# Performance work log

Measured on AMD Instinct MI355X. Metric: run time of the kernel, lower is better.

The kernel has to match this reference:

```python
import jax, jax.numpy as jnp
import numpy as np

B, C, IC, H, W = 4, 256, 128, 64, 64
EPS = 1e-5  # BatchNorm eps (eval mode, running stats)


def conv_bn(x, w, b, gamma, beta, mean, var, relu):
    # 1x1 conv == channel contraction; BN in eval mode (affine w/ running stats)
    y = jnp.einsum('oc,bchw->bohw', w, x) + b[None, :, None, None]
    scale = gamma * jax.lax.rsqrt(var + EPS)
    shift = beta - mean * scale
    y = y * scale[None, :, None, None] + shift[None, :, None, None]
    return jax.nn.relu(y) if relu else y


def setup_inputs() -> dict:
    key = jax.random.key(0)
    ks = jax.random.split(key, 32)

    def branch(i, co, ci):
        return dict(
            w=jax.random.normal(ks[i], (co, ci), jnp.float32) * 0.05,
            b=jax.random.normal(ks[i + 1], (co,), jnp.float32) * 0.05,
            gamma=jax.random.uniform(ks[i + 2], (co,), jnp.float32, 0.5, 1.5),
            beta=jax.random.normal(ks[i + 3], (co,), jnp.float32) * 0.05,
            mean=jax.random.normal(ks[i + 4], (co,), jnp.float32) * 0.05,
            var=jax.random.uniform(ks[i + 5], (co,), jnp.float32, 0.5, 1.5),
        )

    g = branch(0, IC, C)
    th = branch(6, IC, C)
    ph = branch(12, IC, C)
    wo = branch(18, C, IC)
    inp = {'x': jax.random.normal(ks[24], (B, C, H, W), jnp.float32)}
    for pre, p in (('g', g), ('th', th), ('ph', ph), ('w', wo)):
        for k, v in p.items():
            inp[f'{pre}_{k}'] = v
    return inp


def reference(x, g_w, g_b, g_gamma, g_beta, g_mean, g_var,
              th_w, th_b, th_gamma, th_beta, th_mean, th_var,
              ph_w, ph_b, ph_gamma, ph_beta, ph_mean, ph_var,
              w_w, w_b, w_gamma, w_beta, w_mean, w_var):
    b, c, h, w = x.shape
    ic = g_w.shape[0]
    g_x = conv_bn(x, g_w, g_b, g_gamma, g_beta, g_mean, g_var, True).reshape(b, ic, h * w)     # [b,ic,n]
    theta = conv_bn(x, th_w, th_b, th_gamma, th_beta, th_mean, th_var, True).reshape(b, ic, h * w)
    phi = conv_bn(x, ph_w, ph_b, ph_gamma, ph_beta, ph_mean, ph_var, True).reshape(b, ic, h * w)
    # unscaled attention over flattened spatial positions
    f = jnp.einsum('bcn,bcm->bnm', theta, phi)     # [b,n,n]
    a = jax.nn.softmax(f, axis=2)
    y = jnp.einsum('bnm,bcm->bcn', a, g_x)         # [b,ic,n]
    y = y.reshape(b, ic, h, w)
    y = conv_bn(y, w_w, w_b, w_gamma, w_beta, w_mean, w_var, False)
    return y + x
```

## Files before the change

kernel.cpp:

```cpp
#include <hip/hip_runtime.h>
#include <math.h>

typedef __attribute__((ext_vector_type(8))) short short8;
typedef __attribute__((ext_vector_type(8))) _Float16 half8;
typedef __attribute__((ext_vector_type(4))) float f32x4;

#define NSP 4096
#define CIN 256
#define ICH 128
#define SPLITS 4
#define TILES_PER_SPLIT 16
#define LOG2E 1.44269504088896f

__device__ __forceinline__ unsigned short f2h(float x){
  union { _Float16 h; unsigned short u; } v; v.h = (_Float16)x; return v.u;
}
__device__ __forceinline__ float h2f(unsigned short u){
  union { _Float16 h; unsigned short u; } v; v.u = u; return (float)v.h;
}
__device__ __forceinline__ unsigned pk2h(float a, float b){
  union { __fp16 __attribute__((ext_vector_type(2))) v; unsigned u; } r;
  r.v = __builtin_amdgcn_cvt_pkrtz(a, b);
  return r.u;
}
__device__ __forceinline__ float fexp2(float x){
  float r;
  asm("v_exp_f32 %0, %1" : "=v"(r) : "v"(x));
  return r;
}
__device__ __forceinline__ int swz(int row, int e){ return e ^ ((row & 7) << 3); }

__device__ __forceinline__ f32x4 mfmah(short8 a, short8 b, f32x4 c){
  union { short8 s; half8 h; } ua, ub; ua.s = a; ub.s = b;
  return __builtin_amdgcn_mfma_f32_16x16x32_f16(ua.h, ub.h, c, 0, 0, 0);
}

__device__ __forceinline__ void st4h(unsigned short* p, unsigned short a, unsigned short b,
                                     unsigned short c, unsigned short d){
  ushort4 v; v.x=a; v.y=b; v.z=c; v.w=d;
  *(ushort4*)p = v;
}

__device__ __forceinline__ void gload_lds16(const unsigned short* g, unsigned short* l){
  __builtin_amdgcn_global_load_lds(
      (const __attribute__((address_space(1))) unsigned int*)g,
      (__attribute__((address_space(3))) unsigned int*)l, 16, 0, 0);
}

__device__ __forceinline__ void stage_nc(const unsigned short* gbase, unsigned short* lds,
                                         int w, int l){
  #pragma unroll
  for (int i=0;i<4;++i){
    int rl = 16*w + 4*i + (l>>4);
    int eg = ((l&15)*8) ^ ((rl&7)<<3);
    gload_lds16(gbase + (size_t)rl*128 + eg, lds + w*2048 + i*512);
  }
}

__device__ __forceinline__ int kperm(int q){
  return ((q>>4)&1)*4 + ((q>>2)&3)*8 + (q&3);
}

__global__ __launch_bounds__(256) void conv_fused_k(
    const float* __restrict__ x,
    const float* __restrict__ w0, const float* __restrict__ b0,
    const float* __restrict__ ga0, const float* __restrict__ be0,
    const float* __restrict__ me0, const float* __restrict__ va0,
    const float* __restrict__ w1, const float* __restrict__ b1,
    const float* __restrict__ ga1, const float* __restrict__ be1,
    const float* __restrict__ me1, const float* __restrict__ va1,
    const float* __restrict__ w2, const float* __restrict__ b2,
    const float* __restrict__ ga2, const float* __restrict__ be2,
    const float* __restrict__ me2, const float* __restrict__ va2,
    unsigned short* __restrict__ outg, unsigned short* __restrict__ outt,
    unsigned short* __restrict__ outp)
{
  const int b = blockIdx.z, nt = blockIdx.x, ot = blockIdx.y;
  const int n0 = nt*64, o0 = ot*64;
  const int t = threadIdx.x, w = t>>6, l = t&63;
  __shared__ unsigned short xs[64][64];
  __shared__ unsigned short ws[3][64][64];
  __shared__ float sc_s[3][64], sh_s[3][64];
  if (t < 64){
    int o = o0 + t;
    float s0 = ga0[o]*rsqrtf(va0[o]+1e-5f);
    sc_s[0][t]=s0; sh_s[0][t]=be0[o]-me0[o]*s0+b0[o]*s0;
    float s1 = ga1[o]*rsqrtf(va1[o]+1e-5f);
    sc_s[1][t]=s1*LOG2E; sh_s[1][t]=(be1[o]-me1[o]*s1+b1[o]*s1)*LOG2E;
    float s2 = ga2[o]*rsqrtf(va2[o]+1e-5f);
    sc_s[2][t]=s2; sh_s[2][t]=be2[o]-me2[o]*s2+b2[o]*s2;
  }
  const f32x4 Z = {0.f,0.f,0.f,0.f};
  f32x4 acc[3][4];
  #pragma unroll
  for (int br=0;br<3;++br) for (int i=0;i<4;++i) acc[br][i] = Z;
  const float* Wt[3] = {w0, w1, w2};

  for (int kc = 0; kc < CIN; kc += 64){
    __syncthreads();
    #pragma unroll
    for (int p = 0; p < 4; ++p){
      int cw = p*16 + (t>>4);
      int q4 = (t&15)*4;
      float4 xv = *(const float4*)(x + ((size_t)b*CIN + kc + cw)*NSP + n0 + q4);
      float xa[4] = {xv.x, xv.y, xv.z, xv.w};
      #pragma unroll
      for (int i=0;i<4;++i){
        int r = q4 + i;
        xs[r][swz(r, cw)] = f2h(xa[i]);
      }
      #pragma unroll
      for (int br=0;br<3;++br){
        float4 wv = *(const float4*)(Wt[br] + (size_t)(o0 + cw)*CIN + kc + q4);
        int cs = swz(cw, q4);
        st4h(&ws[br][cw][cs], f2h(wv.x), f2h(wv.y), f2h(wv.z), f2h(wv.w));
      }
    }
    __syncthreads();
    #pragma unroll
    for (int kf = 0; kf < 2; ++kf){
      int ko = kf*32 + (l>>4)*8;
      int wr = 16*w + (l&15);
      short8 wf0 = *(const short8*)&ws[0][wr][swz(wr, ko)];
      short8 wf1 = *(const short8*)&ws[1][wr][swz(wr, ko)];
      short8 wf2 = *(const short8*)&ws[2][wr][swz(wr, ko)];
      #pragma unroll
      for (int nf = 0; nf < 4; ++nf){
        int xr = 16*nf + (l&15);
        short8 xf = *(const short8*)&xs[xr][swz(xr, ko)];
        acc[0][nf] = mfmah(wf0, xf, acc[0][nf]);
        acc[1][nf] = mfmah(xf, wf1, acc[1][nf]);
        acc[2][nf] = mfmah(xf, wf2, acc[2][nf]);
      }
    }
  }
  #pragma unroll
  for (int j=0;j<4;++j){
    int ol = 16*w + (l>>4)*4 + j;
    float s = sc_s[0][ol], sh = sh_s[0][ol];
    #pragma unroll
    for (int nf=0;nf<4;++nf){
      int n = n0 + 16*nf + (l&15);
      int nst = (n & ~31) | kperm(n & 31);
      float v = fmaxf(acc[0][nf][j]*s + sh, 0.f);
      outg[((size_t)b*ICH + o0 + ol)*NSP + nst] = f2h(v);
    }
  }
  {
    int ol = 16*w + (l&15);
    float s1 = sc_s[1][ol], sh1 = sh_s[1][ol];
    float s2 = sc_s[2][ol], sh2 = sh_s[2][ol];
    #pragma unroll
    for (int nf=0; nf<4; ++nf)
      #pragma unroll
      for (int j=0;j<4;++j){
        int n = n0 + 16*nf + (l>>4)*4 + j;
        float v1 = fmaxf(acc[1][nf][j]*s1 + sh1, 0.f);
        float v2 = fmaxf(acc[2][nf][j]*s2 + sh2, 0.f);
        outt[((size_t)b*NSP + n)*ICH + o0 + ol] = f2h(v1);
        outp[((size_t)b*NSP + n)*ICH + o0 + ol] = f2h(v2);
      }
  }
}

__global__ __launch_bounds__(256, 2) void attn_k(
  const unsigned short* __restrict__ thp, const unsigned short* __restrict__ php,
  const unsigned short* __restrict__ gb, unsigned short* __restrict__ ypart,
  float* __restrict__ ml)
{
  const int bx = blockIdx.x;
  const int xcd = bx & 7, jj = bx >> 3;
  const int combo = xcd*2 + (jj>>5);
  const int qt = jj & 31;
  const int b = combo & 3, s = combo >> 2;
  const int n0 = qt*128;
  const int t = threadIdx.x, w = t>>6, l = t&63;

  __shared__ unsigned short kb[2][64][128];
  __shared__ unsigned short vb[2][128][64];

  stage_nc(thp + ((size_t)b*NSP + n0      )*ICH, &kb[0][0][0], w, l);
  stage_nc(thp + ((size_t)b*NSP + n0 + 64 )*ICH, &kb[1][0][0], w, l);
  __syncthreads();
  short8 qf0[4], qf1[4];
  {
    int qr = 16*w + (l&15);
    #pragma unroll
    for (int kf=0;kf<4;++kf){
      int ko = kf*32 + (l>>4)*8;
      qf0[kf] = *(const short8*)&kb[0][qr][swz(qr, ko)];
      qf1[kf] = *(const short8*)&kb[1][qr][swz(qr, ko)];
    }
  }
  __syncthreads();

  const f32x4 Z = {0.f,0.f,0.f,0.f};
  f32x4 oa0[8], oa1[8];
  #pragma unroll
  for (int i=0;i<8;++i){ oa0[i]=Z; oa1[i]=Z; }
  float m0r = -1e30f, m1r = -1e30f;
  float l0r = 0.f, l1r = 0.f;
  unsigned pk0[8], pk1[8];

  const int tile0 = s*TILES_PER_SPLIT;

  const unsigned short* kp[4];
  const unsigned short* vp[4];
  {
    const unsigned short* kbase = php + ((size_t)b*NSP + tile0*64)*ICH;
    const unsigned short* vbase = gb + (size_t)b*ICH*NSP + tile0*64;
    #pragma unroll
    for (int i=0;i<4;++i){
      int rl = 16*w + 4*i + (l>>4);
      int eg = ((l&15)*8) ^ ((rl&7)<<3);
      kp[i] = kbase + (size_t)rl*128 + eg;
      int cl = 32*w + 8*i + (l>>3);
      int me = ((l&7)*8) ^ ((cl&7)<<3);
      vp[i] = vbase + (size_t)cl*NSP + me;
    }
  }
  {
    unsigned short* kd = &kb[0][0][0] + w*2048;
    unsigned short* vd = &vb[0][0][0] + w*2048;
    #pragma unroll
    for (int i=0;i<4;++i){
      gload_lds16(kp[i], kd + i*512); kp[i] += 64*ICH;
      gload_lds16(vp[i], vd + i*512); vp[i] += 64;
    }
  }
  __syncthreads();
  int cur = 0;

  for (int it = 0; it < TILES_PER_SPLIT; ++it){
    if (it < TILES_PER_SPLIT-1){
      unsigned short* kd = &kb[cur^1][0][0] + w*2048;
      unsigned short* vd = &vb[cur^1][0][0] + w*2048;
      #pragma unroll
      for (int i=0;i<4;++i){
        gload_lds16(kp[i], kd + i*512); kp[i] += 64*ICH;
        gload_lds16(vp[i], vd + i*512); vp[i] += 64;
      }
    }

    f32x4 f0[4], f1[4];
    #pragma unroll
    for (int i=0;i<4;++i){ f0[i]=Z; f1[i]=Z; }
    __builtin_amdgcn_s_setprio(1);
    #pragma unroll
    for (int mf=0; mf<4; ++mf){
      int kr = 16*mf + (l&15);
      #pragma unroll
      for (int kf=0; kf<4; ++kf){
        short8 bh = *(const short8*)&kb[cur][kr][swz(kr, kf*32 + (l>>4)*8)];
        f0[mf] = mfmah(bh, qf0[kf], f0[mf]);
        f1[mf] = mfmah(bh, qf1[kf], f1[mf]);
      }
    }
    __builtin_amdgcn_s_setprio(0);

    #pragma unroll
    for (int h=0; h<2; ++h){
      f32x4* f = h ? f1 : f0;
      float& mr = h ? m1r : m0r;
      float& lr = h ? l1r : l0r;
      f32x4* oa = h ? oa1 : oa0;
      unsigned* pk = h ? pk1 : pk0;
      float a0 = fmaxf(fmaxf(f[0][0], f[0][1]), fmaxf(f[0][2], f[0][3]));
      float a1 = fmaxf(fmaxf(f[1][0], f[1][1]), fmaxf(f[1][2], f[1][3]));
      float a2 = fmaxf(fmaxf(f[2][0], f[2][1]), fmaxf(f[2][2], f[2][3]));
      float a3 = fmaxf(fmaxf(f[3][0], f[3][1]), fmaxf(f[3][2], f[3][3]));
      float mx = fmaxf(fmaxf(a0, a1), fmaxf(a2, a3));
      mx = fmaxf(mx, __shfl_xor(mx, 16));
      mx = fmaxf(mx, __shfl_xor(mx, 32));
      if (__any(mx - mr > 11.5f)){
        float mn = fmaxf(mr, mx);
        float al = fexp2(mr - mn);
        mr = mn; lr *= al;
        #pragma unroll
        for (int j=0;j<4;++j){
          float alj = __shfl(al, (l>>4)*4 + j);
          #pragma unroll
          for (int cf=0;cf<8;++cf) oa[cf][j] *= alj;
        }
      }
      float s0 = 0.f, s1 = 0.f, s2 = 0.f, s3 = 0.f;
      #pragma unroll
      for (int mf=0;mf<4;++mf){
        float p0 = fexp2(f[mf][0] - mr);
        float p1 = fexp2(f[mf][1] - mr);
        float p2 = fexp2(f[mf][2] - mr);
        float p3 = fexp2(f[mf][3] - mr);
        pk[2*mf+0] = pk2h(p0, p1);
        pk[2*mf+1] = pk2h(p2, p3);
        s0 += p0; s1 += p1; s2 += p2; s3 += p3;
      }
      lr += (s0 + s1) + (s2 + s3);
    }

    __builtin_amdgcn_s_setprio(1);
    {
      int g8 = (l>>4)*8;
      #pragma unroll
      for (int mk=0;mk<2;++mk){
        union { unsigned u[4]; short8 s8; } a0u, a1u;
        #pragma unroll
        for (int q=0;q<4;++q){ a0u.u[q] = pk0[4*mk+q]; a1u.u[q] = pk1[4*mk+q]; }
        #pragma unroll
        for (int cf=0;cf<8;++cf){
          int vr = 16*cf + (l&15);
          short8 bv = *(const short8*)&vb[cur][vr][swz(vr, mk*32 + g8)];
          oa0[cf] = mfmah(a0u.s8, bv, oa0[cf]);
          oa1[cf] = mfmah(a1u.s8, bv, oa1[cf]);
        }
      }
    }
    __builtin_amdgcn_s_setprio(0);

    __syncthreads();
    cur ^= 1;
  }

  #pragma unroll
  for (int h=0; h<2; ++h){
    float mr = h ? m1r : m0r;
    float lr = h ? l1r : l0r;
    f32x4* oa = h ? oa1 : oa0;
    lr += __shfl_xor(lr, 16);
    lr += __shfl_xor(lr, 32);
    float invl = 1.f / lr;
    #pragma unroll
    for (int j=0;j<4;++j){
      float inv = __shfl(invl, (l>>4)*4 + j);
      int n = n0 + h*64 + 16*w + (l>>4)*4 + j;
      #pragma unroll
      for (int cf=0;cf<8;++cf){
        int c = 16*cf + (l&15);
        ypart[(((size_t)s*4 + b)*NSP + n)*ICH + c] = f2h(oa[cf][j]*inv);
      }
    }
    if (l < 16){
      int n = n0 + h*64 + 16*w + l;
      ml[(((size_t)s*4 + b)*NSP + n)*2 + 0] = mr;
      ml[(((size_t)s*4 + b)*NSP + n)*2 + 1] = lr;
    }
  }
}

__global__ __launch_bounds__(256) void final_k(
  const unsigned short* __restrict__ ypart, const float* __restrict__ ml,
  const float* __restrict__ x, const float* __restrict__ Wm,
  const float* __restrict__ bias, const float* __restrict__ gamma,
  const float* __restrict__ beta, const float* __restrict__ mean,
  const float* __restrict__ var, float* __restrict__ out)
{
  const int b = blockIdx.z, ot = blockIdx.y, nt = blockIdx.x;
  const int n0 = nt*64, o0 = ot*64;
  const int t = threadIdx.x, w = t>>6, l = t&63;
  __shared__ unsigned short ys[64][128];
  __shared__ unsigned short w2s[64][128];
  __shared__ float wc[SPLITS][64];
  __shared__ float sc_s[64], sh_s[64];
  if (t < 64){
    int o = o0 + t;
    float s = gamma[o]*rsqrtf(var[o]+1e-5f);
    sc_s[t]=s; sh_s[t]=beta[o]-mean[o]*s+bias[o]*s;
  } else if (t < 128){
    int r = t - 64, n = n0 + r;
    float mv[SPLITS], lv[SPLITS];
    #pragma unroll
    for (int s=0;s<SPLITS;++s){
      mv[s] = ml[(((size_t)s*4 + b)*NSP + n)*2 + 0];
      lv[s] = ml[(((size_t)s*4 + b)*NSP + n)*2 + 1];
    }
    float M = fmaxf(fmaxf(mv[0],mv[1]), fmaxf(mv[2],mv[3]));
    float wsum = 0.f, wv[SPLITS];
    #pragma unroll
    for (int s=0;s<SPLITS;++s){ wv[s] = lv[s]*exp2f(mv[s]-M); wsum += wv[s]; }
    float inv = 1.f/wsum;
    #pragma unroll
    for (int s=0;s<SPLITS;++s) wc[s][r] = wv[s]*inv;
  }
  __syncthreads();
  #pragma unroll
  for (int p=0;p<4;++p){
    int id = p*256 + t, r = id>>4, c8 = (id&15)*8;
    float accv[8] = {0,0,0,0,0,0,0,0};
    #pragma unroll
    for (int s=0;s<SPLITS;++s){
      short8 v = *(const short8*)(ypart + (((size_t)s*4 + b)*NSP + n0 + r)*ICH + c8);
      float wgt = wc[s][r];
      #pragma unroll
      for (int i=0;i<8;++i) accv[i] += wgt * h2f(((unsigned short*)&v)[i]);
    }
    unsigned short hv[8];
    #pragma unroll
    for (int i=0;i<8;++i) hv[i] = f2h(accv[i]);
    *(short8*)&ys[r][swz(r,c8)] = *(short8*)hv;

    float4 u0 = *(const float4*)(Wm + (size_t)(o0 + r)*ICH + c8);
    float4 u1 = *(const float4*)(Wm + (size_t)(o0 + r)*ICH + c8 + 4);
    unsigned short wh[8] = {f2h(u0.x),f2h(u0.y),f2h(u0.z),f2h(u0.w),
                            f2h(u1.x),f2h(u1.y),f2h(u1.z),f2h(u1.w)};
    *(short8*)&w2s[r][swz(r,c8)] = *(short8*)wh;
  }
  __syncthreads();
  const f32x4 Z = {0.f,0.f,0.f,0.f};
  f32x4 acc[4];
  for (int i=0;i<4;++i) acc[i]=Z;
  #pragma unroll
  for (int kf=0;kf<4;++kf){
    int ko = kf*32 + (l>>4)*8;
    int wr = 16*w + (l&15);
    short8 a = *(const short8*)&w2s[wr][swz(wr,ko)];
    #pragma unroll
    for (int nf=0;nf<4;++nf){
      int yr = 16*nf + (l&15);
      short8 bb = *(const short8*)&ys[yr][swz(yr,ko)];
      acc[nf] = mfmah(a, bb, acc[nf]);
    }
  }
  #pragma unroll
  for (int j=0;j<4;++j){
    int ol = 16*w + (l>>4)*4 + j;
    float s = sc_s[ol], sh = sh_s[ol];
    #pragma unroll
    for (int nf=0;nf<4;++nf){
      int n = n0 + 16*nf + (l&15);
      size_t idx = ((size_t)b*CIN + o0 + ol)*NSP + n;
      out[idx] = acc[nf][j]*s + sh + x[idx];
    }
  }
}

extern "C" void kernel_launch(void* const* d_in, const int* in_sizes, int n_in,
                              void* d_out, int out_size, void* d_ws, size_t ws_size,
                              hipStream_t stream){
  const float* x    = (const float*)d_in[0];
  const float* g_w  = (const float*)d_in[1];
  const float* g_b  = (const float*)d_in[2];
  const float* g_ga = (const float*)d_in[3];
  const float* g_be = (const float*)d_in[4];
  const float* g_me = (const float*)d_in[5];
  const float* g_va = (const float*)d_in[6];
  const float* t_w  = (const float*)d_in[7];
  const float* t_b  = (const float*)d_in[8];
  const float* t_ga = (const float*)d_in[9];
  const float* t_be = (const float*)d_in[10];
  const float* t_me = (const float*)d_in[11];
  const float* t_va = (const float*)d_in[12];
  const float* p_w  = (const float*)d_in[13];
  const float* p_b  = (const float*)d_in[14];
  const float* p_ga = (const float*)d_in[15];
  const float* p_be = (const float*)d_in[16];
  const float* p_me = (const float*)d_in[17];
  const float* p_va = (const float*)d_in[18];
  const float* w_w  = (const float*)d_in[19];
  const float* w_b  = (const float*)d_in[20];
  const float* w_ga = (const float*)d_in[21];
  const float* w_be = (const float*)d_in[22];
  const float* w_me = (const float*)d_in[23];
  const float* w_va = (const float*)d_in[24];

  char* ws = (char*)d_ws;
  const size_t SEG = (size_t)4*NSP*ICH*sizeof(unsigned short);
  unsigned short* th_t  = (unsigned short*)(ws);
  unsigned short* ph_t  = (unsigned short*)(ws + SEG);
  unsigned short* g_cn  = (unsigned short*)(ws + 2*SEG);
  unsigned short* ypart = (unsigned short*)(ws + 3*SEG);
  float*          mlb   = (float*)(ws + 3*SEG + SPLITS*SEG);

  dim3 blk(256,1,1);
  conv_fused_k<<<dim3(64,2,4), blk, 0, stream>>>(
      x,
      g_w, g_b, g_ga, g_be, g_me, g_va,
      t_w, t_b, t_ga, t_be, t_me, t_va,
      p_w, p_b, p_ga, p_be, p_me, p_va,
      g_cn, th_t, ph_t);
  attn_k<<<dim3(512,1,1), blk, 0, stream>>>(th_t, ph_t, g_cn, ypart, mlb);
  final_k<<<dim3(64,4,4), blk, 0, stream>>>(ypart, mlb, x, w_w, w_b, w_ga, w_be, w_me, w_va, (float*)d_out);
}
```

Baseline: 71.34 us.

## Template attention kernel on waves per block; use 8-wave blocks with 8 KV splits

The attention kernel is parameterized by waves per block. With enough workspace it launches 512 blocks of 512 threads, each covering 256 query rows and an 8-way split of the key sequence, so each block runs 8 tiles instead of 16. The final combine kernel is templated on the split count so it can merge 8 partial results. More splits and larger blocks mean each K/V tile staged in LDS serves twice as many query rows and the grid carries more waves, at the cost of double the partial-output traffic and a heavier combine step.

```diff
diff --git a/kernel.cpp b/kernel.cpp
--- a/kernel.cpp
+++ b/kernel.cpp
@@ -8,8 +8,6 @@
 #define NSP 4096
 #define CIN 256
 #define ICH 128
-#define SPLITS 4
-#define TILES_PER_SPLIT 16
 #define LOG2E 1.44269504088896f
 
 __device__ __forceinline__ unsigned short f2h(float x){
@@ -45,16 +43,6 @@
   __builtin_amdgcn_global_load_lds(
       (const __attribute__((address_space(1))) unsigned int*)g,
       (__attribute__((address_space(3))) unsigned int*)l, 16, 0, 0);
-}
-
-__device__ __forceinline__ void stage_nc(const unsigned short* gbase, unsigned short* lds,
-                                         int w, int l){
-  #pragma unroll
-  for (int i=0;i<4;++i){
-    int rl = 16*w + 4*i + (l>>4);
-    int eg = ((l&15)*8) ^ ((rl&7)<<3);
-    gload_lds16(gbase + (size_t)rl*128 + eg, lds + w*2048 + i*512);
-  }
 }
 
 __device__ __forceinline__ int kperm(int q){
@@ -163,33 +151,62 @@
   }
 }
 
-__global__ __launch_bounds__(256, 2) void attn_k(
+template<int WPB>
+__global__ __launch_bounds__(WPB*64, WPB/2) void attn_k(
   const unsigned short* __restrict__ thp, const unsigned short* __restrict__ php,
   const unsigned short* __restrict__ gb, unsigned short* __restrict__ ypart,
   float* __restrict__ ml)
 {
+  constexpr int QROWS = WPB*32;
+  constexpr int HBLK  = WPB*16;
+  constexpr int TPS   = 64/WPB;
+  constexpr int QTC   = 128/WPB;
+  constexpr int NLD   = 16/WPB;
+
   const int bx = blockIdx.x;
   const int xcd = bx & 7, jj = bx >> 3;
-  const int combo = xcd*2 + (jj>>5);
-  const int qt = jj & 31;
+  const int combo = xcd*(WPB/2) + jj/QTC;
+  const int qt = jj % QTC;
   const int b = combo & 3, s = combo >> 2;
-  const int n0 = qt*128;
+  const int n0 = qt*QROWS;
   const int t = threadIdx.x, w = t>>6, l = t&63;
 
-  __shared__ unsigned short kb[2][64][128];
-  __shared__ unsigned short vb[2][128][64];
-
-  stage_nc(thp + ((size_t)b*NSP + n0      )*ICH, &kb[0][0][0], w, l);
-  stage_nc(thp + ((size_t)b*NSP + n0 + 64 )*ICH, &kb[1][0][0], w, l);
+  __shared__ unsigned short kbuf[2][8192];
+  __shared__ unsigned short vbuf[2][8192];
+
+  unsigned short* kb0 = kbuf[0];
+  unsigned short* kb1 = kbuf[1];
+  unsigned short* vb0 = vbuf[0];
+  unsigned short* vb1 = vbuf[1];
+  auto qsel = [&](int c) -> unsigned short* {
+    return c==0 ? kb0 : (c==1 ? kb1 : (c==2 ? vb0 : vb1));
+  };
+
+  #pragma unroll
+  for (int c=0;c<WPB/2;++c){
+    const unsigned short* src = thp + ((size_t)b*NSP + n0 + c*64)*ICH;
+    unsigned short* dst = qsel(c) + w*(NLD*512);
+    #pragma unroll
+    for (int i=0;i<NLD;++i){
+      int rl = (64/WPB)*w + 4*i + (l>>4);
+      int eg = ((l&15)*8) ^ ((rl&7)<<3);
+      gload_lds16(src + (size_t)rl*128 + eg, dst + i*512);
+    }
+  }
   __syncthreads();
   short8 qf0[4], qf1[4];
   {
-    int qr = 16*w + (l&15);
+    int base0 = 16*w;
+    int c0 = base0>>6, r0 = (base0&63) + (l&15);
+    int base1 = HBLK + 16*w;
+    int c1 = base1>>6, r1 = (base1&63) + (l&15);
+    unsigned short* p0 = qsel(c0);
+    unsigned short* p1 = qsel(c1);
     #pragma unroll
     for (int kf=0;kf<4;++kf){
       int ko = kf*32 + (l>>4)*8;
-      qf0[kf] = *(const short8*)&kb[0][qr][swz(qr, ko)];
-      qf1[kf] = *(const short8*)&kb[1][qr][swz(qr, ko)];
+      qf0[kf] = *(const short8*)&p0[r0*128 + swz(r0, ko)];
+      qf1[kf] = *(const short8*)&p1[r1*128 + swz(r1, ko)];
     }
   }
   __syncthreads();
@@ -202,28 +219,28 @@
   float l0r = 0.f, l1r = 0.f;
   unsigned pk0[8], pk1[8];
 
-  const int tile0 = s*TILES_PER_SPLIT;
-
-  const unsigned short* kp[4];
-  const unsigned short* vp[4];
+  const int tile0 = s*TPS;
+
+  const unsigned short* kp[NLD];
+  const unsigned short* vp[NLD];
   {
     const unsigned short* kbase = php + ((size_t)b*NSP + tile0*64)*ICH;
     const unsigned short* vbase = gb + (size_t)b*ICH*NSP + tile0*64;
     #pragma unroll
-    for (int i=0;i<4;++i){
-      int rl = 16*w + 4*i + (l>>4);
+    for (int i=0;i<NLD;++i){
+      int rl = (64/WPB)*w + 4*i + (l>>4);
       int eg = ((l&15)*8) ^ ((rl&7)<<3);
       kp[i] = kbase + (size_t)rl*128 + eg;
-      int cl = 32*w + 8*i + (l>>3);
+      int cl = (128/WPB)*w + 8*i + (l>>3);
       int me = ((l&7)*8) ^ ((cl&7)<<3);
       vp[i] = vbase + (size_t)cl*NSP + me;
     }
   }
   {
-    unsigned short* kd = &kb[0][0][0] + w*2048;
-    unsigned short* vd = &vb[0][0][0] + w*2048;
-    #pragma unroll
-    for (int i=0;i<4;++i){
+    unsigned short* kd = kb0 + w*(NLD*512);
+    unsigned short* vd = vb0 + w*(NLD*512);
+    #pragma unroll
+    for (int i=0;i<NLD;++i){
       gload_lds16(kp[i], kd + i*512); kp[i] += 64*ICH;
       gload_lds16(vp[i], vd + i*512); vp[i] += 64;
     }
@@ -231,12 +248,14 @@
   __syncthreads();
   int cur = 0;
 
-  for (int it = 0; it < TILES_PER_SPLIT; ++it){
-    if (it < TILES_PER_SPLIT-1){
-      unsigned short* kd = &kb[cur^1][0][0] + w*2048;
-      unsigned short* vd = &vb[cur^1][0][0] + w*2048;
-      #pragma unroll
-      for (int i=0;i<4;++i){
+  for (int it = 0; it < TPS; ++it){
+    unsigned short* kcur = cur ? kb1 : kb0;
+    unsigned short* vcur = cur ? vb1 : vb0;
+    if (it < TPS-1){
+      unsigned short* kd = (cur ? kb0 : kb1) + w*(NLD*512);
+      unsigned short* vd = (cur ? vb0 : vb1) + w*(NLD*512);
+      #pragma unroll
+      for (int i=0;i<NLD;++i){
         gload_lds16(kp[i], kd + i*512); kp[i] += 64*ICH;
         gload_lds16(vp[i], vd + i*512); vp[i] += 64;
       }
@@ -251,7 +270,7 @@
       int kr = 16*mf + (l&15);
       #pragma unroll
       for (int kf=0; kf<4; ++kf){
-        short8 bh = *(const short8*)&kb[cur][kr][swz(kr, kf*32 + (l>>4)*8)];
+        short8 bh = *(const short8*)&kcur[kr*128 + swz(kr, kf*32 + (l>>4)*8)];
         f0[mf] = mfmah(bh, qf0[kf], f0[mf]);
         f1[mf] = mfmah(bh, qf1[kf], f1[mf]);
       }
@@ -308,7 +327,7 @@
         #pragma unroll
         for (int cf=0;cf<8;++cf){
           int vr = 16*cf + (l&15);
-          short8 bv = *(const short8*)&vb[cur][vr][swz(vr, mk*32 + g8)];
+          short8 bv = *(const short8*)&vcur[vr*64 + swz(vr, mk*32 + g8)];
           oa0[cf] = mfmah(a0u.s8, bv, oa0[cf]);
           oa1[cf] = mfmah(a1u.s8, bv, oa1[cf]);
         }
@@ -331,7 +350,7 @@
     #pragma unroll
     for (int j=0;j<4;++j){
       float inv = __shfl(invl, (l>>4)*4 + j);
-      int n = n0 + h*64 + 16*w + (l>>4)*4 + j;
+      int n = n0 + h*HBLK + 16*w + (l>>4)*4 + j;
       #pragma unroll
       for (int cf=0;cf<8;++cf){
         int c = 16*cf + (l&15);
@@ -339,13 +358,14 @@
       }
     }
     if (l < 16){
-      int n = n0 + h*64 + 16*w + l;
+      int n = n0 + h*HBLK + 16*w + l;
       ml[(((size_t)s*4 + b)*NSP + n)*2 + 0] = mr;
       ml[(((size_t)s*4 + b)*NSP + n)*2 + 1] = lr;
     }
   }
 }
 
+template<int SPL>
 __global__ __launch_bounds__(256) void final_k(
   const unsigned short* __restrict__ ypart, const float* __restrict__ ml,
   const float* __restrict__ x, const float* __restrict__ Wm,
@@ -358,7 +378,7 @@
   const int t = threadIdx.x, w = t>>6, l = t&63;
   __shared__ unsigned short ys[64][128];
   __shared__ unsigned short w2s[64][128];
-  __shared__ float wc[SPLITS][64];
+  __shared__ float wc[SPL][64];
   __shared__ float sc_s[64], sh_s[64];
   if (t < 64){
     int o = o0 + t;
@@ -366,19 +386,21 @@
     sc_s[t]=s; sh_s[t]=beta[o]-mean[o]*s+bias[o]*s;
   } else if (t < 128){
     int r = t - 64, n = n0 + r;
-    float mv[SPLITS], lv[SPLITS];
-    #pragma unroll
-    for (int s=0;s<SPLITS;++s){
+    float mv[SPL], lv[SPL];
+    #pragma unroll
+    for (int s=0;s<SPL;++s){
       mv[s] = ml[(((size_t)s*4 + b)*NSP + n)*2 + 0];
       lv[s] = ml[(((size_t)s*4 + b)*NSP + n)*2 + 1];
     }
-    float M = fmaxf(fmaxf(mv[0],mv[1]), fmaxf(mv[2],mv[3]));
-    float wsum = 0.f, wv[SPLITS];
-    #pragma unroll
-    for (int s=0;s<SPLITS;++s){ wv[s] = lv[s]*exp2f(mv[s]-M); wsum += wv[s]; }
+    float M = mv[0];
+    #pragma unroll
+    for (int s=1;s<SPL;++s) M = fmaxf(M, mv[s]);
+    float wsum = 0.f, wv[SPL];
+    #pragma unroll
+    for (int s=0;s<SPL;++s){ wv[s] = lv[s]*exp2f(mv[s]-M); wsum += wv[s]; }
     float inv = 1.f/wsum;
     #pragma unroll
-    for (int s=0;s<SPLITS;++s) wc[s][r] = wv[s]*inv;
+    for (int s=0;s<SPL;++s) wc[s][r] = wv[s]*inv;
   }
   __syncthreads();
   #pragma unroll
@@ -386,7 +408,7 @@
     int id = p*256 + t, r = id>>4, c8 = (id&15)*8;
     float accv[8] = {0,0,0,0,0,0,0,0};
     #pragma unroll
-    for (int s=0;s<SPLITS;++s){
+    for (int s=0;s<SPL;++s){
       short8 v = *(const short8*)(ypart + (((size_t)s*4 + b)*NSP + n0 + r)*ICH + c8);
       float wgt = wc[s][r];
       #pragma unroll
@@ -463,11 +485,13 @@
 
   char* ws = (char*)d_ws;
   const size_t SEG = (size_t)4*NSP*ICH*sizeof(unsigned short);
+  const size_t MLSZ8 = (size_t)8*4*NSP*2*sizeof(float);
+  const size_t NEED8 = 3*SEG + 8*SEG + MLSZ8;
+
   unsigned short* th_t  = (unsigned short*)(ws);
   unsigned short* ph_t  = (unsigned short*)(ws + SEG);
   unsigned short* g_cn  = (unsigned short*)(ws + 2*SEG);
   unsigned short* ypart = (unsigned short*)(ws + 3*SEG);
-  float*          mlb   = (float*)(ws + 3*SEG + SPLITS*SEG);
 
   dim3 blk(256,1,1);
   conv_fused_k<<<dim3(64,2,4), blk, 0, stream>>>(
@@ -476,6 +500,14 @@
       t_w, t_b, t_ga, t_be, t_me, t_va,
       p_w, p_b, p_ga, p_be, p_me, p_va,
       g_cn, th_t, ph_t);
-  attn_k<<<dim3(512,1,1), blk, 0, stream>>>(th_t, ph_t, g_cn, ypart, mlb);
-  final_k<<<dim3(64,4,4), blk, 0, stream>>>(ypart, mlb, x, w_w, w_b, w_ga, w_be, w_me, w_va, (float*)d_out);
-}
+
+  if (ws_size >= NEED8){
+    float* mlb = (float*)(ws + 3*SEG + 8*SEG);
+    attn_k<8><<<dim3(512,1,1), dim3(512,1,1), 0, stream>>>(th_t, ph_t, g_cn, ypart, mlb);
+    final_k<8><<<dim3(64,4,4), blk, 0, stream>>>(ypart, mlb, x, w_w, w_b, w_ga, w_be, w_me, w_va, (float*)d_out);
+  } else {
+    float* mlb = (float*)(ws + 3*SEG + 4*SEG);
+    attn_k<4><<<dim3(512,1,1), blk, 0, stream>>>(th_t, ph_t, g_cn, ypart, mlb);
+    final_k<4><<<dim3(64,4,4), blk, 0, stream>>>(ypart, mlb, x, w_w, w_b, w_ga, w_be, w_me, w_va, (float*)d_out);
+  }
+}
```

Result: slower. 146.1 us (+104.9%).

## Use eight KV splits, single-buffer V in LDS, raise attention occupancy

Applied to the files above, without the earlier changes.

The attention kernel becomes a template over the split count. When the workspace is large enough it launches 1024 blocks with 8 splits of 8 tiles each, which gives more parallelism across the CUs. V is now single-buffered: it is loaded at the start of each iteration and waited on with an explicit vmcnt plus a barrier before the PV MFMAs, which frees LDS so the launch bound can target 3 blocks per CU. The trade-offs are more partial outputs to write and merge in final_k, exposed V load latency inside each iteration, and possible register pressure at the higher occupancy.

```diff
diff --git a/kernel.cpp b/kernel.cpp
--- a/kernel.cpp
+++ b/kernel.cpp
@@ -8,8 +8,6 @@
 #define NSP 4096
 #define CIN 256
 #define ICH 128
-#define SPLITS 4
-#define TILES_PER_SPLIT 16
 #define LOG2E 1.44269504088896f
 
 __device__ __forceinline__ unsigned short f2h(float x){
@@ -163,21 +161,24 @@
   }
 }
 
-__global__ __launch_bounds__(256, 2) void attn_k(
+template<int SPLITS_T>
+__global__ __launch_bounds__(256, 3) void attn_k(
   const unsigned short* __restrict__ thp, const unsigned short* __restrict__ php,
   const unsigned short* __restrict__ gb, unsigned short* __restrict__ ypart,
   float* __restrict__ ml)
 {
+  constexpr int TPS = 64/SPLITS_T;
   const int bx = blockIdx.x;
   const int xcd = bx & 7, jj = bx >> 3;
-  const int combo = xcd*2 + (jj>>5);
-  const int qt = jj & 31;
+  const int combo = xcd*(SPLITS_T/2) + jj/32;
+  const int qt = jj % 32;
   const int b = combo & 3, s = combo >> 2;
   const int n0 = qt*128;
   const int t = threadIdx.x, w = t>>6, l = t&63;
 
   __shared__ unsigned short kb[2][64][128];
-  __shared__ unsigned short vb[2][128][64];
+  __shared__ unsigned short vb[128][64];
+  unsigned short* vbf = &vb[0][0];
 
   stage_nc(thp + ((size_t)b*NSP + n0      )*ICH, &kb[0][0][0], w, l);
   stage_nc(thp + ((size_t)b*NSP + n0 + 64 )*ICH, &kb[1][0][0], w, l);
@@ -202,7 +203,7 @@
   float l0r = 0.f, l1r = 0.f;
   unsigned pk0[8], pk1[8];
 
-  const int tile0 = s*TILES_PER_SPLIT;
+  const int tile0 = s*TPS;
 
   const unsigned short* kp[4];
   const unsigned short* vp[4];
@@ -221,24 +222,27 @@
   }
   {
     unsigned short* kd = &kb[0][0][0] + w*2048;
-    unsigned short* vd = &vb[0][0][0] + w*2048;
     #pragma unroll
     for (int i=0;i<4;++i){
       gload_lds16(kp[i], kd + i*512); kp[i] += 64*ICH;
-      gload_lds16(vp[i], vd + i*512); vp[i] += 64;
     }
   }
   __syncthreads();
   int cur = 0;
 
-  for (int it = 0; it < TILES_PER_SPLIT; ++it){
-    if (it < TILES_PER_SPLIT-1){
+  for (int it = 0; it < TPS; ++it){
+    {
+      unsigned short* vd = vbf + w*2048;
+      #pragma unroll
+      for (int i=0;i<4;++i){
+        gload_lds16(vp[i], vd + i*512); vp[i] += 64;
+      }
+    }
+    if (it < TPS-1){
       unsigned short* kd = &kb[cur^1][0][0] + w*2048;
-      unsigned short* vd = &vb[cur^1][0][0] + w*2048;
       #pragma unroll
       for (int i=0;i<4;++i){
         gload_lds16(kp[i], kd + i*512); kp[i] += 64*ICH;
-        gload_lds16(vp[i], vd + i*512); vp[i] += 64;
       }
     }
 
@@ -297,6 +301,13 @@
       lr += (s0 + s1) + (s2 + s3);
     }
 
+    if (it < TPS-1)
+      asm volatile("s_waitcnt vmcnt(4)" ::: "memory");
+    else
+      asm volatile("s_waitcnt vmcnt(0)" ::: "memory");
+    __builtin_amdgcn_s_barrier();
+    __builtin_amdgcn_sched_barrier(0);
+
     __builtin_amdgcn_s_setprio(1);
     {
       int g8 = (l>>4)*8;
@@ -308,7 +319,7 @@
         #pragma unroll
         for (int cf=0;cf<8;++cf){
           int vr = 16*cf + (l&15);
-          short8 bv = *(const short8*)&vb[cur][vr][swz(vr, mk*32 + g8)];
+          short8 bv = *(const short8*)&vbf[vr*64 + swz(vr, mk*32 + g8)];
           oa0[cf] = mfmah(a0u.s8, bv, oa0[cf]);
           oa1[cf] = mfmah(a1u.s8, bv, oa1[cf]);
         }
@@ -346,6 +357,7 @@
   }
 }
 
+template<int SPL>
 __global__ __launch_bounds__(256) void final_k(
   const unsigned short* __restrict__ ypart, const float* __restrict__ ml,
   const float* __restrict__ x, const float* __restrict__ Wm,
@@ -358,7 +370,7 @@
   const int t = threadIdx.x, w = t>>6, l = t&63;
   __shared__ unsigned short ys[64][128];
   __shared__ unsigned short w2s[64][128];
-  __shared__ float wc[SPLITS][64];
+  __shared__ float wc[SPL][64];
   __shared__ float sc_s[64], sh_s[64];
   if (t < 64){
     int o = o0 + t;
@@ -366,19 +378,21 @@
     sc_s[t]=s; sh_s[t]=beta[o]-mean[o]*s+bias[o]*s;
   } else if (t < 128){
     int r = t - 64, n = n0 + r;
-    float mv[SPLITS], lv[SPLITS];
-    #pragma unroll
-    for (int s=0;s<SPLITS;++s){
+    float mv[SPL], lv[SPL];
+    #pragma unroll
+    for (int s=0;s<SPL;++s){
       mv[s] = ml[(((size_t)s*4 + b)*NSP + n)*2 + 0];
       lv[s] = ml[(((size_t)s*4 + b)*NSP + n)*2 + 1];
     }
-    float M = fmaxf(fmaxf(mv[0],mv[1]), fmaxf(mv[2],mv[3]));
-    float wsum = 0.f, wv[SPLITS];
-    #pragma unroll
-    for (int s=0;s<SPLITS;++s){ wv[s] = lv[s]*exp2f(mv[s]-M); wsum += wv[s]; }
+    float M = mv[0];
+    #pragma unroll
+    for (int s=1;s<SPL;++s) M = fmaxf(M, mv[s]);
+    float wsum = 0.f, wv[SPL];
+    #pragma unroll
+    for (int s=0;s<SPL;++s){ wv[s] = lv[s]*exp2f(mv[s]-M); wsum += wv[s]; }
     float inv = 1.f/wsum;
     #pragma unroll
-    for (int s=0;s<SPLITS;++s) wc[s][r] = wv[s]*inv;
+    for (int s=0;s<SPL;++s) wc[s][r] = wv[s]*inv;
   }
   __syncthreads();
   #pragma unroll
@@ -386,7 +400,7 @@
     int id = p*256 + t, r = id>>4, c8 = (id&15)*8;
     float accv[8] = {0,0,0,0,0,0,0,0};
     #pragma unroll
-    for (int s=0;s<SPLITS;++s){
+    for (int s=0;s<SPL;++s){
       short8 v = *(const short8*)(ypart + (((size_t)s*4 + b)*NSP + n0 + r)*ICH + c8);
       float wgt = wc[s][r];
       #pragma unroll
@@ -463,11 +477,13 @@
 
   char* ws = (char*)d_ws;
   const size_t SEG = (size_t)4*NSP*ICH*sizeof(unsigned short);
+  const size_t MLSZ8 = (size_t)8*4*NSP*2*sizeof(float);
+  const size_t NEED8 = 3*SEG + 8*SEG + MLSZ8;
+
   unsigned short* th_t  = (unsigned short*)(ws);
   unsigned short* ph_t  = (unsigned short*)(ws + SEG);
   unsigned short* g_cn  = (unsigned short*)(ws + 2*SEG);
   unsigned short* ypart = (unsigned short*)(ws + 3*SEG);
-  float*          mlb   = (float*)(ws + 3*SEG + SPLITS*SEG);
 
   dim3 blk(256,1,1);
   conv_fused_k<<<dim3(64,2,4), blk, 0, stream>>>(
@@ -476,6 +492,14 @@
       t_w, t_b, t_ga, t_be, t_me, t_va,
       p_w, p_b, p_ga, p_be, p_me, p_va,
       g_cn, th_t, ph_t);
-  attn_k<<<dim3(512,1,1), blk, 0, stream>>>(th_t, ph_t, g_cn, ypart, mlb);
-  final_k<<<dim3(64,4,4), blk, 0, stream>>>(ypart, mlb, x, w_w, w_b, w_ga, w_be, w_me, w_va, (float*)d_out);
-}
+
+  if (ws_size >= NEED8){
+    float* mlb = (float*)(ws + 3*SEG + 8*SEG);
+    attn_k<8><<<dim3(1024,1,1), blk, 0, stream>>>(th_t, ph_t, g_cn, ypart, mlb);
+    final_k<8><<<dim3(64,4,4), blk, 0, stream>>>(ypart, mlb, x, w_w, w_b, w_ga, w_be, w_me, w_va, (float*)d_out);
+  } else {
+    float* mlb = (float*)(ws + 3*SEG + 4*SEG);
+    attn_k<4><<<dim3(512,1,1), blk, 0, stream>>>(th_t, ph_t, g_cn, ypart, mlb);
+    final_k<4><<<dim3(64,4,4), blk, 0, stream>>>(ypart, mlb, x, w_w, w_b, w_ga, w_be, w_me, w_va, (float*)d_out);
+  }
+}
```

After: 82.62 us. +15.8%, slower.
